# Kernel optimization log

Hardware: AMD Instinct MI355X
Metric: run time of the kernel (lower is better)

The kernel has to match this reference:

```python
import jax, jax.numpy as jnp
import numpy as np

B, L, D = 4096, 50, 128          # users, neighbors/user, embed_dim
N_U, N_I, N_R, N_T = 10000, 100000, 6, 1000
EPS = 1e-5                       # BatchNorm eps (eval mode, running stats)


def setup_inputs() -> dict:
    key = jax.random.key(0)
    ks = iter(jax.random.split(key, 80))
    nk = lambda: next(ks)

    def lin(din, dout):
        s = 1.0 / np.sqrt(din)
        w = jax.random.uniform(nk(), (din, dout), minval=-s, maxval=s, dtype=jnp.float32)
        b = jax.random.uniform(nk(), (dout,), minval=-s, maxval=s, dtype=jnp.float32)
        return w, b

    inp = {}
    # embedding tables (u2e/i2e/r2e/t2e)
    inp['u2e'] = 0.1 * jax.random.normal(nk(), (N_U, D), jnp.float32)
    inp['i2e'] = 0.1 * jax.random.normal(nk(), (N_I, D), jnp.float32)
    inp['r2e'] = 0.1 * jax.random.normal(nk(), (N_R, D), jnp.float32)
    inp['t2e'] = 0.1 * jax.random.normal(nk(), (N_T, D), jnp.float32)
    # neighbor transform MLP
    inp['ne_w'], inp['ne_b'] = lin(3 * D, D)
    inp['ne1_w'], inp['ne1_b'] = lin(D, D)
    # attention MLP (NewAttention: concat(neigh, user) -> D -> D -> 1, softmax over neighbors)
    inp['att1_w'], inp['att1_b'] = lin(2 * D, D)
    inp['att2_w'], inp['att2_b'] = lin(D, D)
    inp['att3_w'], inp['att3_b'] = lin(D, 1)
    # head
    inp['lin_w'], inp['lin_b'] = lin(2 * D, D)
    inp['w1_w'], inp['w1_b'] = lin(D, D // 4)
    inp['bn1_g'] = jnp.ones((D // 4,), jnp.float32)
    inp['bn1_b'] = jnp.zeros((D // 4,), jnp.float32)
    inp['bn1_m'] = 0.1 * jax.random.normal(nk(), (D // 4,), jnp.float32)
    inp['bn1_v'] = jax.random.uniform(nk(), (D // 4,), minval=0.5, maxval=1.5, dtype=jnp.float32)
    inp['w2_w'], inp['w2_b'] = lin(D // 4, D // 8)
    inp['bn2_g'] = jnp.ones((D // 8,), jnp.float32)
    inp['bn2_b'] = jnp.zeros((D // 8,), jnp.float32)
    inp['bn2_m'] = 0.1 * jax.random.normal(nk(), (D // 8,), jnp.float32)
    inp['bn2_v'] = jax.random.uniform(nk(), (D // 8,), minval=0.5, maxval=1.5, dtype=jnp.float32)
    inp['w3_w'], inp['w3_b'] = lin(D // 8, 1)
    # index inputs (padded-fixed neighbor lists)
    inp['user_idx'] = jax.random.randint(nk(), (B,), 0, N_U)
    inp['item_idx'] = jax.random.randint(nk(), (B, L), 0, N_I)
    inp['rat_idx'] = jax.random.randint(nk(), (B, L), 0, N_R)
    inp['time_idx'] = jax.random.randint(nk(), (B, L), 0, N_T)
    return inp


def reference(u2e, i2e, r2e, t2e, ne_w, ne_b, ne1_w, ne1_b,
              att1_w, att1_b, att2_w, att2_b, att3_w, att3_b,
              lin_w, lin_b, w1_w, w1_b, bn1_g, bn1_b, bn1_m, bn1_v,
              w2_w, w2_b, bn2_g, bn2_b, bn2_m, bn2_v, w3_w, w3_b,
              user_idx, item_idx, rat_idx, time_idx):
    u = u2e[user_idx]                                                   # [B, D]
    neigh = jnp.concatenate([i2e[item_idx], r2e[rat_idx], t2e[time_idx]], axis=-1)  # [B, L, 3D]
    x = jax.nn.relu(neigh @ ne_w + ne_b)                                # [B, L, D]
    x = jax.nn.relu(x @ ne1_w + ne1_b)                                  # [B, L, D]
    # attention over neighbors, conditioned on the user embedding
    a = jnp.concatenate([x, jnp.broadcast_to(u[:, None, :], x.shape)], axis=-1)  # [B, L, 2D]
    a = jax.nn.relu(a @ att1_w + att1_b)
    a = jax.nn.relu(a @ att2_w + att2_b)
    att = jax.nn.softmax((a @ att3_w + att3_b)[..., 0], axis=-1)        # [B, L]
    pooled = jnp.einsum('bl,bld->bd', att, x)                           # torch.mm(x.t(), att).t()
    comb = jax.nn.relu(jnp.concatenate([u, pooled], axis=-1) @ lin_w + lin_b)  # [B, D]
    h = comb @ w1_w + w1_b
    h = jax.nn.relu((h - bn1_m) * jax.lax.rsqrt(bn1_v + EPS) * bn1_g + bn1_b)
    h = h @ w2_w + w2_b
    h = jax.nn.relu((h - bn2_m) * jax.lax.rsqrt(bn2_v + EPS) * bn2_g + bn2_b)
    return (h @ w3_w + w3_b)[:, 0]                                      # [B]
```

## Files before the change

kernel.cpp:

```cpp
#include <hip/hip_runtime.h>
#include <hip/hip_bf16.h>

typedef __bf16 bf16x8 __attribute__((ext_vector_type(8)));
typedef float  f32x4  __attribute__((ext_vector_type(4)));

#define W_OFF 0
#define A_OFF 16384
#define X_OFF 29696
#define SMALL 43008
#define SMEM_TOTAL 47104
#define WCHUNK 16384
#define WHALF  8192

#define WS_WPREP 0
#define WS_PI    262144
#define WS_PT    (WS_PI + 25600000)
#define WS_PR    (WS_PT + 512000)
#define WS_PU    (WS_PR + 3072)
#define WS_PU2   (WS_PU + 5120000)

__global__ void prep_weights_kernel(const float* __restrict__ ne_w,
                                    const float* __restrict__ ne1_w,
                                    const float* __restrict__ att1_w,
                                    const float* __restrict__ att2_w,
                                    const float* __restrict__ lin_w,
                                    __hip_bfloat16* __restrict__ wout) {
  __shared__ float tile[64][65];
  const int bx = blockIdx.x;
  const int c = bx >> 2, kt = (bx >> 1) & 1, ntile = bx & 1;
  const float* src; int koff;
  if      (c < 3)  { src = ne_w;   koff = c * 128; }
  else if (c == 3) { src = ne1_w;  koff = 0; }
  else if (c == 4) { src = att1_w; koff = 0; }
  else if (c == 5) { src = att2_w; koff = 0; }
  else if (c == 6) { src = att1_w; koff = 128; }
  else             { src = lin_w;  koff = 0; }
  const int tx = threadIdx.x, ty = threadIdx.y;
#pragma unroll
  for (int r = 0; r < 16; ++r) {
    int k = kt * 64 + r * 4 + ty, n = ntile * 64 + tx;
    tile[r * 4 + ty][tx] = src[(koff + k) * 128 + n];
  }
  __syncthreads();
#pragma unroll
  for (int r = 0; r < 16; ++r) {
    int n = ntile * 64 + r * 4 + ty, k = kt * 64 + tx;
    int h = k >> 6, k64 = k & 63;
    int off = c * WCHUNK + h * WHALF + n * 64 + ((((k64 >> 3) ^ (n & 7))) << 3) + (k64 & 7);
    wout[off] = __float2bfloat16(tile[tx][r * 4 + ty]);
  }
}

__device__ __forceinline__ unsigned short bf_bits(float x) {
  return __builtin_bit_cast(unsigned short, __float2bfloat16(x));
}

__device__ __forceinline__ void mfma_half(const __hip_bfloat16* sIn,
                                          const __hip_bfloat16* sWh,
                                          f32x4 acc[4], int h, int m16, int nh, int lane) {
  const int mr = lane & 15;
  const int kq = lane >> 4;
  const int arow = (m16 * 16 + mr) * 128;
#pragma unroll
  for (int ks = 0; ks < 2; ++ks) {
    const int kb16 = h * 8 + ks * 4 + kq;
    bf16x8 a = *(const bf16x8*)(sIn + arow + ((kb16 ^ mr) << 3));
    const int swzb = (((ks * 4 + kq) ^ (mr & 7)) << 3);
#pragma unroll
    for (int nt = 0; nt < 4; ++nt) {
      const int n = nh * 64 + nt * 16 + mr;
      bf16x8 b = *(const bf16x8*)(sWh + n * 64 + swzb);
      acc[nt] = __builtin_amdgcn_mfma_f32_16x16x32_bf16(a, b, acc[nt], 0, 0, 0);
    }
  }
}

__device__ __forceinline__ void epilogue(f32x4 acc[4], const float* __restrict__ bias,
                                         const float* addvec, __hip_bfloat16* sOut,
                                         int m16, int nh, int lane) {
  const int mr = lane & 15;
  const int rb = m16 * 16 + ((lane >> 4) << 2);
#pragma unroll
  for (int nt = 0; nt < 4; ++nt) {
    const int col = nh * 64 + nt * 16 + mr;
    float bv = bias[col];
    if (addvec) bv += addvec[col];
    const int cblk = col >> 3, clo = col & 7;
#pragma unroll
    for (int r = 0; r < 4; ++r) {
      const int row = rb + r;
      if (row < 50) {
        float v = fmaxf(acc[nt][r] + bv, 0.0f);
        sOut[row * 128 + ((cblk ^ (row & 15)) << 3) + clo] = __float2bfloat16(v);
      }
    }
  }
}

__global__ __launch_bounds__(512) void pgemm_kernel(
    const float* __restrict__ i2e, const float* __restrict__ r2e,
    const float* __restrict__ t2e, const float* __restrict__ u2e,
    const float* __restrict__ ne_b, const __hip_bfloat16* __restrict__ wprep,
    __hip_bfloat16* __restrict__ Pi, float* __restrict__ Pt, float* __restrict__ Pr,
    float* __restrict__ Pu, float* __restrict__ Pu2) {
  __shared__ __align__(16) __hip_bfloat16 sW[WCHUNK];
  __shared__ __align__(16) __hip_bfloat16 sA[64 * 128];
  const int tid = threadIdx.x, lane = tid & 63, wid = tid >> 6;
  const int m16 = wid & 3, nh = wid >> 2;
  const int bx = blockIdx.x;
  const float* src; const __hip_bfloat16* W; float* dst = nullptr;
  const float* addb = nullptr; bool bf_out = false;
  long rows0; int nrows;
  if (bx < 1563)      { src = i2e; W = wprep + 0 * WCHUNK; bf_out = true; rows0 = (long)bx * 64;          nrows = 100000; }
  else if (bx < 1579) { src = t2e; W = wprep + 2 * WCHUNK; dst = Pt;  rows0 = (long)(bx - 1563) * 64; nrows = 1000; }
  else if (bx < 1580) { src = r2e; W = wprep + 1 * WCHUNK; dst = Pr;  rows0 = 0;                      nrows = 6; addb = ne_b; }
  else if (bx < 1737) { src = u2e; W = wprep + 6 * WCHUNK; dst = Pu;  rows0 = (long)(bx - 1580) * 64; nrows = 10000; }
  else                { src = u2e; W = wprep + 7 * WCHUNK; dst = Pu2; rows0 = (long)(bx - 1737) * 64; nrows = 10000; }

#pragma unroll
  for (int i = 0; i < 4; ++i) {
    int g = tid + i * 512;
    __builtin_amdgcn_global_load_lds(
        (__attribute__((address_space(1))) void*)(void*)(W + g * 8),
        (__attribute__((address_space(3))) void*)(void*)(sW + g * 8), 16, 0, 0);
  }
  const float4* s4 = (const float4*)src;
#pragma unroll
  for (int i = 0; i < 2; ++i) {
    int g = tid + i * 512;
    int row = g >> 4, kb = g & 15;
    float4 v0 = {0.f, 0.f, 0.f, 0.f}, v1 = {0.f, 0.f, 0.f, 0.f};
    if (rows0 + row < nrows) {
      long base = (rows0 + row) * 32 + kb * 2;
      v0 = s4[base]; v1 = s4[base + 1];
    }
    uint4 pk;
    pk.x = ((unsigned)bf_bits(v0.y) << 16) | bf_bits(v0.x);
    pk.y = ((unsigned)bf_bits(v0.w) << 16) | bf_bits(v0.z);
    pk.z = ((unsigned)bf_bits(v1.y) << 16) | bf_bits(v1.x);
    pk.w = ((unsigned)bf_bits(v1.w) << 16) | bf_bits(v1.z);
    *(uint4*)(sA + row * 128 + ((kb ^ (row & 15)) << 3)) = pk;
  }
  __syncthreads();

  f32x4 acc[4];
#pragma unroll
  for (int j = 0; j < 4; ++j) acc[j] = (f32x4){0.f, 0.f, 0.f, 0.f};
  mfma_half(sA, sW, acc, 0, m16, nh, lane);
  mfma_half(sA, sW + WHALF, acc, 1, m16, nh, lane);

  const int mr = lane & 15;
  const int rb = m16 * 16 + ((lane >> 4) << 2);
#pragma unroll
  for (int nt = 0; nt < 4; ++nt) {
    const int col = nh * 64 + nt * 16 + mr;
    const float bv = addb ? addb[col] : 0.f;
#pragma unroll
    for (int r = 0; r < 4; ++r) {
      const int row = rb + r;
      if (rows0 + row < nrows) {
        if (bf_out) Pi[(rows0 + row) * 128 + col] = __float2bfloat16(acc[nt][r]);
        else        dst[(rows0 + row) * 128 + col] = acc[nt][r] + bv;
      }
    }
  }
}

__global__ __launch_bounds__(512, 6) void graphdec_main(
    const __hip_bfloat16* __restrict__ Pi, const float* __restrict__ Pt,
    const float* __restrict__ Pr, const float* __restrict__ Pu,
    const float* __restrict__ Pu2,
    const float* __restrict__ ne1_b, const float* __restrict__ att1_b,
    const float* __restrict__ att2_b, const float* __restrict__ att3_w,
    const float* __restrict__ lin_w, const float* __restrict__ lin_b,
    const float* __restrict__ w1_w, const float* __restrict__ w1_b,
    const float* __restrict__ bn1_g, const float* __restrict__ bn1_b,
    const float* __restrict__ bn1_m, const float* __restrict__ bn1_v,
    const float* __restrict__ w2_w, const float* __restrict__ w2_b,
    const float* __restrict__ bn2_g, const float* __restrict__ bn2_b,
    const float* __restrict__ bn2_m, const float* __restrict__ bn2_v,
    const float* __restrict__ w3_w, const float* __restrict__ w3_b,
    const int* __restrict__ user_idx, const int* __restrict__ item_idx,
    const int* __restrict__ rat_idx, const int* __restrict__ time_idx,
    const __hip_bfloat16* __restrict__ wprep, float* __restrict__ out) {
  __shared__ __align__(16) unsigned char smem[SMEM_TOTAL];
  __hip_bfloat16* sW = (__hip_bfloat16*)(smem + W_OFF);
  __hip_bfloat16* sA = (__hip_bfloat16*)(smem + A_OFF);
  __hip_bfloat16* sX = (__hip_bfloat16*)(smem + X_OFF);
  int*   sIdx   = (int*)  (smem + SMALL);
  float* sUatt  = (float*)(smem + SMALL + 768);
  float* sUlin  = (float*)(smem + SMALL + 1280);
  float* sLP0   = (float*)(smem + SMALL + 1792);
  float* sLP1   = (float*)(smem + SMALL + 2048);
  float* sAtt   = (float*)(smem + SMALL + 2304);
  float* sPooled= (float*)(smem + SMALL + 2560);
  float* sComb  = (float*)(smem + SMALL + 3072);
  float* sH1    = (float*)(smem + SMALL + 3584);
  float* sPool4 = (float*)(smem + W_OFF);
  float* sCombP = (float*)(smem + W_OFF + 2048);

  const int tid  = threadIdx.x;
  const int lane = tid & 63;
  const int wid  = tid >> 6;
  const int m16  = wid & 3;
  const int nh   = wid >> 2;
  const int b    = blockIdx.x;

  float att3r[4];
#pragma unroll
  for (int nt = 0; nt < 4; ++nt) att3r[nt] = att3_w[nh * 64 + nt * 16 + (lane & 15)];

  if (tid < 192) {
    int c = tid >> 6, l = tid & 63;
    int v = 0;
    if (l < 50) {
      const int* p = (c == 0) ? item_idx : (c == 1) ? rat_idx : time_idx;
      v = p[b * 50 + l];
    }
    sIdx[tid] = v;
  }
  const int uid = user_idx[b];
  if (tid >= 256 && tid < 384)      sUatt[tid - 256] = Pu [(long)uid * 128 + (tid - 256)];
  else if (tid >= 384)              sUlin[tid - 384] = Pu2[(long)uid * 128 + (tid - 384)];
  __syncthreads();

  auto stage16 = [&](const __hip_bfloat16* __restrict__ src) {
#pragma unroll
    for (int i = 0; i < 2; ++i) {
      int g = tid + i * 512;
      __builtin_amdgcn_global_load_lds(
          (__attribute__((address_space(1))) void*)(void*)(src + g * 8),
          (__attribute__((address_space(3))) void*)(void*)(sW + g * 8), 16, 0, 0);
    }
  };

  f32x4 acc[4];
  const f32x4 zf = {0.f, 0.f, 0.f, 0.f};
  auto zacc = [&]() {
#pragma unroll
    for (int j = 0; j < 4; ++j) acc[j] = zf;
  };

  stage16(wprep + 3 * WCHUNK);
#pragma unroll
  for (int i = 0; i < 2; ++i) {
    int g = tid + i * 512;
    if (g < 832) {
      int row = g >> 4, kb = g & 15;
      uint4 pk = {0u, 0u, 0u, 0u};
      if (row < 50) {
        const bf16x8 pv = *(const bf16x8*)(Pi + (long)sIdx[row] * 128 + kb * 8);
        const float4* pr4 = (const float4*)(Pr + (long)sIdx[64 + row] * 128) + kb * 2;
        const float4* pt4 = (const float4*)(Pt + (long)sIdx[128 + row] * 128) + kb * 2;
        float4 r0 = pr4[0], r1 = pr4[1];
        float4 t0 = pt4[0], t1 = pt4[1];
        float s0 = fmaxf((float)pv[0] + r0.x + t0.x, 0.f);
        float s1 = fmaxf((float)pv[1] + r0.y + t0.y, 0.f);
        float s2 = fmaxf((float)pv[2] + r0.z + t0.z, 0.f);
        float s3 = fmaxf((float)pv[3] + r0.w + t0.w, 0.f);
        float s4 = fmaxf((float)pv[4] + r1.x + t1.x, 0.f);
        float s5 = fmaxf((float)pv[5] + r1.y + t1.y, 0.f);
        float s6 = fmaxf((float)pv[6] + r1.z + t1.z, 0.f);
        float s7 = fmaxf((float)pv[7] + r1.w + t1.w, 0.f);
        pk.x = ((unsigned)bf_bits(s1) << 16) | bf_bits(s0);
        pk.y = ((unsigned)bf_bits(s3) << 16) | bf_bits(s2);
        pk.z = ((unsigned)bf_bits(s5) << 16) | bf_bits(s4);
        pk.w = ((unsigned)bf_bits(s7) << 16) | bf_bits(s6);
      }
      *(uint4*)(sA + row * 128 + ((kb ^ (row & 15)) << 3)) = pk;
    }
  }
  __syncthreads();

  zacc();
  mfma_half(sA, sW, acc, 0, m16, nh, lane);
  __syncthreads();
  stage16(wprep + 3 * WCHUNK + WHALF);
  __syncthreads();
  mfma_half(sA, sW, acc, 1, m16, nh, lane);
  __syncthreads();
  stage16(wprep + 4 * WCHUNK);
  epilogue(acc, ne1_b, nullptr, sX, m16, nh, lane);
  __syncthreads();

  zacc();
  mfma_half(sX, sW, acc, 0, m16, nh, lane);
  __syncthreads();
  stage16(wprep + 4 * WCHUNK + WHALF);
  __syncthreads();
  mfma_half(sX, sW, acc, 1, m16, nh, lane);
  __syncthreads();
  stage16(wprep + 5 * WCHUNK);
  epilogue(acc, att1_b, sUatt, sA, m16, nh, lane);
  __syncthreads();

  zacc();
  mfma_half(sA, sW, acc, 0, m16, nh, lane);
  __syncthreads();
  stage16(wprep + 5 * WCHUNK + WHALF);
  __syncthreads();
  mfma_half(sA, sW, acc, 1, m16, nh, lane);
  {
    float lp[4] = {0.f, 0.f, 0.f, 0.f};
#pragma unroll
    for (int nt = 0; nt < 4; ++nt) {
      const int col = nh * 64 + nt * 16 + (lane & 15);
      const float b2 = att2_b[col];
#pragma unroll
      for (int r = 0; r < 4; ++r)
        lp[r] += fmaxf(acc[nt][r] + b2, 0.f) * att3r[nt];
    }
#pragma unroll
    for (int off = 1; off < 16; off <<= 1) {
#pragma unroll
      for (int r = 0; r < 4; ++r) lp[r] += __shfl_xor(lp[r], off);
    }
    if ((lane & 15) == 0) {
      const int rowb = m16 * 16 + ((lane >> 4) << 2);
      float* dst = nh ? sLP1 : sLP0;
#pragma unroll
      for (int r = 0; r < 4; ++r) dst[rowb + r] = lp[r];
    }
  }
  __syncthreads();

  if (wid == 0) {
    float v = (lane < 50) ? (sLP0[lane] + sLP1[lane]) : -3.4e38f;
    float m = v;
    for (int off = 32; off > 0; off >>= 1) m = fmaxf(m, __shfl_xor(m, off));
    float e = (lane < 50) ? __expf(v - m) : 0.f;
    float s = e;
    for (int off = 32; off > 0; off >>= 1) s += __shfl_xor(s, off);
    sAtt[lane] = e / s;
  }
  __syncthreads();

  {
    int q = tid >> 7, d = tid & 127;
    const int cblk = d >> 3, clo = d & 7;
    float s = 0.f;
    for (int l = q; l < 50; l += 4)
      s += sAtt[l] * (float)sX[l * 128 + ((cblk ^ (l & 15)) << 3) + clo];
    sPool4[q * 128 + d] = s;
  }
  __syncthreads();
  if (tid < 128)
    sPooled[tid] = sPool4[tid] + sPool4[128 + tid] + sPool4[256 + tid] + sPool4[384 + tid];
  __syncthreads();

  {
    int q = tid >> 7, d = tid & 127;
    float s = 0.f;
    for (int j = q * 32; j < q * 32 + 32; ++j) s += sPooled[j] * lin_w[(128 + j) * 128 + d];
    sCombP[q * 128 + d] = s;
  }
  __syncthreads();
  if (tid < 128)
    sComb[tid] = fmaxf(sCombP[tid] + sCombP[128 + tid] + sCombP[256 + tid] + sCombP[384 + tid]
                       + sUlin[tid] + lin_b[tid], 0.f);
  __syncthreads();

  if (wid == 0) {
    if (lane < 32) {
      float s = w1_b[lane];
      for (int k = 0; k < 128; ++k) s += sComb[k] * w1_w[k * 32 + lane];
      s = (s - bn1_m[lane]) * rsqrtf(bn1_v[lane] + 1e-5f) * bn1_g[lane] + bn1_b[lane];
      sH1[lane] = fmaxf(s, 0.f);
    }
    if (lane < 16) {
      float s = w2_b[lane];
      for (int k = 0; k < 32; ++k) s += sH1[k] * w2_w[k * 16 + lane];
      s = (s - bn2_m[lane]) * rsqrtf(bn2_v[lane] + 1e-5f) * bn2_g[lane] + bn2_b[lane];
      float p = fmaxf(s, 0.f) * w3_w[lane];
      p += __shfl_xor(p, 1); p += __shfl_xor(p, 2);
      p += __shfl_xor(p, 4); p += __shfl_xor(p, 8);
      if (lane == 0) out[b] = p + w3_b[0];
    }
  }
}

extern "C" void kernel_launch(void* const* d_in, const int* in_sizes, int n_in,
                              void* d_out, int out_size, void* d_ws, size_t ws_size,
                              hipStream_t stream) {
  const float* u2e    = (const float*)d_in[0];
  const float* i2e    = (const float*)d_in[1];
  const float* r2e    = (const float*)d_in[2];
  const float* t2e    = (const float*)d_in[3];
  const float* ne_w   = (const float*)d_in[4];
  const float* ne_b   = (const float*)d_in[5];
  const float* ne1_w  = (const float*)d_in[6];
  const float* ne1_b  = (const float*)d_in[7];
  const float* att1_w = (const float*)d_in[8];
  const float* att1_b = (const float*)d_in[9];
  const float* att2_w = (const float*)d_in[10];
  const float* att2_b = (const float*)d_in[11];
  const float* att3_w = (const float*)d_in[12];
  const float* att3_b = (const float*)d_in[13];
  const float* lin_w  = (const float*)d_in[14];
  const float* lin_b  = (const float*)d_in[15];
  const float* w1_w   = (const float*)d_in[16];
  const float* w1_b   = (const float*)d_in[17];
  const float* bn1_g  = (const float*)d_in[18];
  const float* bn1_b  = (const float*)d_in[19];
  const float* bn1_m  = (const float*)d_in[20];
  const float* bn1_v  = (const float*)d_in[21];
  const float* w2_w   = (const float*)d_in[22];
  const float* w2_b   = (const float*)d_in[23];
  const float* bn2_g  = (const float*)d_in[24];
  const float* bn2_b  = (const float*)d_in[25];
  const float* bn2_m  = (const float*)d_in[26];
  const float* bn2_v  = (const float*)d_in[27];
  const float* w3_w   = (const float*)d_in[28];
  const float* w3_b   = (const float*)d_in[29];
  const int* user_idx = (const int*)d_in[30];
  const int* item_idx = (const int*)d_in[31];
  const int* rat_idx  = (const int*)d_in[32];
  const int* time_idx = (const int*)d_in[33];
  (void)att3_b;

  char* ws = (char*)d_ws;
  __hip_bfloat16* wprep = (__hip_bfloat16*)(ws + WS_WPREP);
  __hip_bfloat16* Pi = (__hip_bfloat16*)(ws + WS_PI);
  float* Pt  = (float*)(ws + WS_PT);
  float* Pr  = (float*)(ws + WS_PR);
  float* Pu  = (float*)(ws + WS_PU);
  float* Pu2 = (float*)(ws + WS_PU2);
  float* out = (float*)d_out;

  prep_weights_kernel<<<32, dim3(64, 4), 0, stream>>>(ne_w, ne1_w, att1_w, att2_w,
                                                      lin_w, wprep);
  pgemm_kernel<<<1894, 512, 0, stream>>>(i2e, r2e, t2e, u2e, ne_b, wprep,
                                         Pi, Pt, Pr, Pu, Pu2);
  graphdec_main<<<4096, 512, 0, stream>>>(
      Pi, Pt, Pr, Pu, Pu2, ne1_b, att1_b, att2_b, att3_w,
      lin_w, lin_b, w1_w, w1_b, bn1_g, bn1_b, bn1_m, bn1_v, w2_w, w2_b,
      bn2_g, bn2_b, bn2_m, bn2_v, w3_w, w3_b,
      user_idx, item_idx, rat_idx, time_idx, wprep, out);
}
```

Baseline: 242.3 us.

## Process two users per 1024-thread block sharing staged weight chunks

Fuses two users into one 1024-thread block. Each half-block gets its own activation, hidden and scratch LDS regions, while the bf16 weight chunk staged into LDS is shared by both, so each weight chunk is loaded once per two users. It also drops the zero-fill of padding rows 50-63 in the gather stage, cutting the activation buffers to 50 rows. The trade-off is a larger LDS footprint per block and a tighter register budget from the launch bounds. Reading the unwritten pad rows could also touch the other user's buffer unless those rows are masked later.

```diff
diff --git a/kernel.cpp b/kernel.cpp
--- a/kernel.cpp
+++ b/kernel.cpp
@@ -5,10 +5,10 @@
 typedef float  f32x4  __attribute__((ext_vector_type(4)));
 
 #define W_OFF 0
-#define A_OFF 16384
-#define X_OFF 29696
-#define SMALL 43008
-#define SMEM_TOTAL 47104
+#define ABUF  16384
+#define XBUF  41984
+#define SMALL 67584
+#define SMEM_TOTAL 75776
 #define WCHUNK 16384
 #define WHALF  8192
 
@@ -166,7 +166,7 @@
   }
 }
 
-__global__ __launch_bounds__(512, 6) void graphdec_main(
+__global__ __launch_bounds__(1024, 8) void graphdec_main(
     const __hip_bfloat16* __restrict__ Pi, const float* __restrict__ Pt,
     const float* __restrict__ Pr, const float* __restrict__ Pu,
     const float* __restrict__ Pu2,
@@ -184,54 +184,54 @@
     const int* __restrict__ rat_idx, const int* __restrict__ time_idx,
     const __hip_bfloat16* __restrict__ wprep, float* __restrict__ out) {
   __shared__ __align__(16) unsigned char smem[SMEM_TOTAL];
-  __hip_bfloat16* sW = (__hip_bfloat16*)(smem + W_OFF);
-  __hip_bfloat16* sA = (__hip_bfloat16*)(smem + A_OFF);
-  __hip_bfloat16* sX = (__hip_bfloat16*)(smem + X_OFF);
-  int*   sIdx   = (int*)  (smem + SMALL);
-  float* sUatt  = (float*)(smem + SMALL + 768);
-  float* sUlin  = (float*)(smem + SMALL + 1280);
-  float* sLP0   = (float*)(smem + SMALL + 1792);
-  float* sLP1   = (float*)(smem + SMALL + 2048);
-  float* sAtt   = (float*)(smem + SMALL + 2304);
-  float* sPooled= (float*)(smem + SMALL + 2560);
-  float* sComb  = (float*)(smem + SMALL + 3072);
-  float* sH1    = (float*)(smem + SMALL + 3584);
-  float* sPool4 = (float*)(smem + W_OFF);
-  float* sCombP = (float*)(smem + W_OFF + 2048);
-
   const int tid  = threadIdx.x;
+  const int t    = tid & 511;
+  const int u    = tid >> 9;
   const int lane = tid & 63;
-  const int wid  = tid >> 6;
+  const int wid  = (tid >> 6) & 7;
   const int m16  = wid & 3;
   const int nh   = wid >> 2;
   const int b    = blockIdx.x;
+  const long ub  = (long)b * 2 + u;
+
+  __hip_bfloat16* sW = (__hip_bfloat16*)(smem + W_OFF);
+  __hip_bfloat16* sA = (__hip_bfloat16*)(smem + ABUF + u * 12800);
+  __hip_bfloat16* sX = (__hip_bfloat16*)(smem + XBUF + u * 12800);
+  unsigned char* sSm = smem + SMALL + u * 4096;
+  int*   sIdx   = (int*)  sSm;
+  float* sUatt  = (float*)(sSm + 768);
+  float* sUlin  = (float*)(sSm + 1280);
+  float* sLP0   = (float*)(sSm + 1792);
+  float* sLP1   = (float*)(sSm + 2048);
+  float* sAtt   = (float*)(sSm + 2304);
+  float* sPooled= (float*)(sSm + 2560);
+  float* sComb  = (float*)(sSm + 3072);
+  float* sH1    = (float*)(sSm + 3584);
+  float* sPool4 = (float*)(smem + W_OFF + u * 4096);
+  float* sCombP = (float*)(smem + W_OFF + u * 4096 + 2048);
 
   float att3r[4];
 #pragma unroll
   for (int nt = 0; nt < 4; ++nt) att3r[nt] = att3_w[nh * 64 + nt * 16 + (lane & 15)];
 
-  if (tid < 192) {
-    int c = tid >> 6, l = tid & 63;
+  if (t < 192) {
+    int c = t >> 6, l = t & 63;
     int v = 0;
     if (l < 50) {
       const int* p = (c == 0) ? item_idx : (c == 1) ? rat_idx : time_idx;
-      v = p[b * 50 + l];
-    }
-    sIdx[tid] = v;
-  }
-  const int uid = user_idx[b];
-  if (tid >= 256 && tid < 384)      sUatt[tid - 256] = Pu [(long)uid * 128 + (tid - 256)];
-  else if (tid >= 384)              sUlin[tid - 384] = Pu2[(long)uid * 128 + (tid - 384)];
+      v = p[ub * 50 + l];
+    }
+    sIdx[t] = v;
+  }
+  const int uid = user_idx[ub];
+  if (t >= 256 && t < 384)      sUatt[t - 256] = Pu [(long)uid * 128 + (t - 256)];
+  else if (t >= 384)            sUlin[t - 384] = Pu2[(long)uid * 128 + (t - 384)];
   __syncthreads();
 
   auto stage16 = [&](const __hip_bfloat16* __restrict__ src) {
-#pragma unroll
-    for (int i = 0; i < 2; ++i) {
-      int g = tid + i * 512;
-      __builtin_amdgcn_global_load_lds(
-          (__attribute__((address_space(1))) void*)(void*)(src + g * 8),
-          (__attribute__((address_space(3))) void*)(void*)(sW + g * 8), 16, 0, 0);
-    }
+    __builtin_amdgcn_global_load_lds(
+        (__attribute__((address_space(1))) void*)(void*)(src + tid * 8),
+        (__attribute__((address_space(3))) void*)(void*)(sW + tid * 8), 16, 0, 0);
   };
 
   f32x4 acc[4];
@@ -244,29 +244,27 @@
   stage16(wprep + 3 * WCHUNK);
 #pragma unroll
   for (int i = 0; i < 2; ++i) {
-    int g = tid + i * 512;
-    if (g < 832) {
+    int g = t + i * 512;
+    if (g < 800) {
       int row = g >> 4, kb = g & 15;
-      uint4 pk = {0u, 0u, 0u, 0u};
-      if (row < 50) {
-        const bf16x8 pv = *(const bf16x8*)(Pi + (long)sIdx[row] * 128 + kb * 8);
-        const float4* pr4 = (const float4*)(Pr + (long)sIdx[64 + row] * 128) + kb * 2;
-        const float4* pt4 = (const float4*)(Pt + (long)sIdx[128 + row] * 128) + kb * 2;
-        float4 r0 = pr4[0], r1 = pr4[1];
-        float4 t0 = pt4[0], t1 = pt4[1];
-        float s0 = fmaxf((float)pv[0] + r0.x + t0.x, 0.f);
-        float s1 = fmaxf((float)pv[1] + r0.y + t0.y, 0.f);
-        float s2 = fmaxf((float)pv[2] + r0.z + t0.z, 0.f);
-        float s3 = fmaxf((float)pv[3] + r0.w + t0.w, 0.f);
-        float s4 = fmaxf((float)pv[4] + r1.x + t1.x, 0.f);
-        float s5 = fmaxf((float)pv[5] + r1.y + t1.y, 0.f);
-        float s6 = fmaxf((float)pv[6] + r1.z + t1.z, 0.f);
-        float s7 = fmaxf((float)pv[7] + r1.w + t1.w, 0.f);
-        pk.x = ((unsigned)bf_bits(s1) << 16) | bf_bits(s0);
-        pk.y = ((unsigned)bf_bits(s3) << 16) | bf_bits(s2);
-        pk.z = ((unsigned)bf_bits(s5) << 16) | bf_bits(s4);
-        pk.w = ((unsigned)bf_bits(s7) << 16) | bf_bits(s6);
-      }
+      const bf16x8 pv = *(const bf16x8*)(Pi + (long)sIdx[row] * 128 + kb * 8);
+      const float4* pr4 = (const float4*)(Pr + (long)sIdx[64 + row] * 128) + kb * 2;
+      const float4* pt4 = (const float4*)(Pt + (long)sIdx[128 + row] * 128) + kb * 2;
+      float4 r0 = pr4[0], r1 = pr4[1];
+      float4 t0 = pt4[0], t1 = pt4[1];
+      float s0 = fmaxf((float)pv[0] + r0.x + t0.x, 0.f);
+      float s1 = fmaxf((float)pv[1] + r0.y + t0.y, 0.f);
+      float s2 = fmaxf((float)pv[2] + r0.z + t0.z, 0.f);
+      float s3 = fmaxf((float)pv[3] + r0.w + t0.w, 0.f);
+      float s4 = fmaxf((float)pv[4] + r1.x + t1.x, 0.f);
+      float s5 = fmaxf((float)pv[5] + r1.y + t1.y, 0.f);
+      float s6 = fmaxf((float)pv[6] + r1.z + t1.z, 0.f);
+      float s7 = fmaxf((float)pv[7] + r1.w + t1.w, 0.f);
+      uint4 pk;
+      pk.x = ((unsigned)bf_bits(s1) << 16) | bf_bits(s0);
+      pk.y = ((unsigned)bf_bits(s3) << 16) | bf_bits(s2);
+      pk.z = ((unsigned)bf_bits(s5) << 16) | bf_bits(s4);
+      pk.w = ((unsigned)bf_bits(s7) << 16) | bf_bits(s6);
       *(uint4*)(sA + row * 128 + ((kb ^ (row & 15)) << 3)) = pk;
     }
   }
@@ -336,7 +334,7 @@
   __syncthreads();
 
   {
-    int q = tid >> 7, d = tid & 127;
+    int q = t >> 7, d = t & 127;
     const int cblk = d >> 3, clo = d & 7;
     float s = 0.f;
     for (int l = q; l < 50; l += 4)
@@ -344,20 +342,20 @@
     sPool4[q * 128 + d] = s;
   }
   __syncthreads();
-  if (tid < 128)
-    sPooled[tid] = sPool4[tid] + sPool4[128 + tid] + sPool4[256 + tid] + sPool4[384 + tid];
+  if (t < 128)
+    sPooled[t] = sPool4[t] + sPool4[128 + t] + sPool4[256 + t] + sPool4[384 + t];
   __syncthreads();
 
   {
-    int q = tid >> 7, d = tid & 127;
+    int q = t >> 7, d = t & 127;
     float s = 0.f;
     for (int j = q * 32; j < q * 32 + 32; ++j) s += sPooled[j] * lin_w[(128 + j) * 128 + d];
     sCombP[q * 128 + d] = s;
   }
   __syncthreads();
-  if (tid < 128)
-    sComb[tid] = fmaxf(sCombP[tid] + sCombP[128 + tid] + sCombP[256 + tid] + sCombP[384 + tid]
-                       + sUlin[tid] + lin_b[tid], 0.f);
+  if (t < 128)
+    sComb[t] = fmaxf(sCombP[t] + sCombP[128 + t] + sCombP[256 + t] + sCombP[384 + t]
+                     + sUlin[t] + lin_b[t], 0.f);
   __syncthreads();
 
   if (wid == 0) {
@@ -374,7 +372,7 @@
       float p = fmaxf(s, 0.f) * w3_w[lane];
       p += __shfl_xor(p, 1); p += __shfl_xor(p, 2);
       p += __shfl_xor(p, 4); p += __shfl_xor(p, 8);
-      if (lane == 0) out[b] = p + w3_b[0];
+      if (lane == 0) out[ub] = p + w3_b[0];
     }
   }
 }
@@ -431,7 +429,7 @@
                                                       lin_w, wprep);
   pgemm_kernel<<<1894, 512, 0, stream>>>(i2e, r2e, t2e, u2e, ne_b, wprep,
                                          Pi, Pt, Pr, Pu, Pu2);
-  graphdec_main<<<4096, 512, 0, stream>>>(
+  graphdec_main<<<2048, 1024, 0, stream>>>(
       Pi, Pt, Pr, Pu, Pu2, ne1_b, att1_b, att2_b, att3_w,
       lin_w, lin_b, w1_w, w1_b, bn1_g, bn1_b, bn1_m, bn1_v, w2_w, w2_b,
       bn2_g, bn2_b, bn2_m, bn2_v, w3_w, w3_b,
```

Result: slower. 283.9 us (+17.2%).

## Process four row tiles per pgemm block with register-prefetched next tile

Applied to the files above, without the earlier changes.

Each pgemm block now loops over up to four 64-row tiles instead of handling one. The weight chunk is loaded into LDS once per block, and the next tile's global loads are issued into registers while the current tile's MFMA and stores run. The aim is to amortize weight staging and block launch overhead and to hide global load latency. In exchange the grid shrinks from 1894 to 476 blocks, which lowers parallelism on a large GPU, and each tile step adds two extra barriers.

```diff
diff --git a/kernel.cpp b/kernel.cpp
--- a/kernel.cpp
+++ b/kernel.cpp
@@ -110,12 +110,14 @@
   const int bx = blockIdx.x;
   const float* src; const __hip_bfloat16* W; float* dst = nullptr;
   const float* addb = nullptr; bool bf_out = false;
-  long rows0; int nrows;
-  if (bx < 1563)      { src = i2e; W = wprep + 0 * WCHUNK; bf_out = true; rows0 = (long)bx * 64;          nrows = 100000; }
-  else if (bx < 1579) { src = t2e; W = wprep + 2 * WCHUNK; dst = Pt;  rows0 = (long)(bx - 1563) * 64; nrows = 1000; }
-  else if (bx < 1580) { src = r2e; W = wprep + 1 * WCHUNK; dst = Pr;  rows0 = 0;                      nrows = 6; addb = ne_b; }
-  else if (bx < 1737) { src = u2e; W = wprep + 6 * WCHUNK; dst = Pu;  rows0 = (long)(bx - 1580) * 64; nrows = 10000; }
-  else                { src = u2e; W = wprep + 7 * WCHUNK; dst = Pu2; rows0 = (long)(bx - 1737) * 64; nrows = 10000; }
+  long rows0; long nrows;
+  if (bx < 391)      { src = i2e; W = wprep + 0 * WCHUNK; bf_out = true; rows0 = (long)bx * 256;        nrows = 100000; }
+  else if (bx < 395) { src = t2e; W = wprep + 2 * WCHUNK; dst = Pt;  rows0 = (long)(bx - 391) * 256; nrows = 1000; }
+  else if (bx < 396) { src = r2e; W = wprep + 1 * WCHUNK; dst = Pr;  rows0 = 0;                      nrows = 6; addb = ne_b; }
+  else if (bx < 436) { src = u2e; W = wprep + 6 * WCHUNK; dst = Pu;  rows0 = (long)(bx - 396) * 256; nrows = 10000; }
+  else               { src = u2e; W = wprep + 7 * WCHUNK; dst = Pu2; rows0 = (long)(bx - 436) * 256; nrows = 10000; }
+  int T = (int)((nrows - rows0 + 63) >> 6);
+  if (T > 4) T = 4;
 
 #pragma unroll
   for (int i = 0; i < 4; ++i) {
@@ -124,44 +126,77 @@
         (__attribute__((address_space(1))) void*)(void*)(W + g * 8),
         (__attribute__((address_space(3))) void*)(void*)(sW + g * 8), 16, 0, 0);
   }
+
   const float4* s4 = (const float4*)src;
-#pragma unroll
-  for (int i = 0; i < 2; ++i) {
-    int g = tid + i * 512;
-    int row = g >> 4, kb = g & 15;
-    float4 v0 = {0.f, 0.f, 0.f, 0.f}, v1 = {0.f, 0.f, 0.f, 0.f};
-    if (rows0 + row < nrows) {
-      long base = (rows0 + row) * 32 + kb * 2;
-      v0 = s4[base]; v1 = s4[base + 1];
-    }
-    uint4 pk;
-    pk.x = ((unsigned)bf_bits(v0.y) << 16) | bf_bits(v0.x);
-    pk.y = ((unsigned)bf_bits(v0.w) << 16) | bf_bits(v0.z);
-    pk.z = ((unsigned)bf_bits(v1.y) << 16) | bf_bits(v1.x);
-    pk.w = ((unsigned)bf_bits(v1.w) << 16) | bf_bits(v1.z);
-    *(uint4*)(sA + row * 128 + ((kb ^ (row & 15)) << 3)) = pk;
-  }
-  __syncthreads();
-
-  f32x4 acc[4];
-#pragma unroll
-  for (int j = 0; j < 4; ++j) acc[j] = (f32x4){0.f, 0.f, 0.f, 0.f};
-  mfma_half(sA, sW, acc, 0, m16, nh, lane);
-  mfma_half(sA, sW + WHALF, acc, 1, m16, nh, lane);
+  const int row = (tid & 511) >> 4;
+
+  auto load_tile = [&](int tt, float4 v[4]) {
+#pragma unroll
+    for (int i = 0; i < 2; ++i) {
+      int g = tid + i * 512;
+      int rr = g >> 4, kb = g & 15;
+      v[i * 2 + 0] = (float4){0.f, 0.f, 0.f, 0.f};
+      v[i * 2 + 1] = (float4){0.f, 0.f, 0.f, 0.f};
+      long gr = rows0 + (long)tt * 64 + rr;
+      if (gr < nrows) {
+        long base = gr * 32 + kb * 2;
+        v[i * 2 + 0] = s4[base];
+        v[i * 2 + 1] = s4[base + 1];
+      }
+    }
+  };
+  auto tile_to_lds = [&](const float4 v[4]) {
+#pragma unroll
+    for (int i = 0; i < 2; ++i) {
+      int g = tid + i * 512;
+      int rr = g >> 4, kb = g & 15;
+      uint4 pk;
+      pk.x = ((unsigned)bf_bits(v[i * 2].y) << 16) | bf_bits(v[i * 2].x);
+      pk.y = ((unsigned)bf_bits(v[i * 2].w) << 16) | bf_bits(v[i * 2].z);
+      pk.z = ((unsigned)bf_bits(v[i * 2 + 1].y) << 16) | bf_bits(v[i * 2 + 1].x);
+      pk.w = ((unsigned)bf_bits(v[i * 2 + 1].w) << 16) | bf_bits(v[i * 2 + 1].z);
+      *(uint4*)(sA + rr * 128 + ((kb ^ (rr & 15)) << 3)) = pk;
+    }
+  };
+  (void)row;
+
+  {
+    float4 cur[4];
+    load_tile(0, cur);
+    tile_to_lds(cur);
+  }
+  __syncthreads();
 
   const int mr = lane & 15;
   const int rb = m16 * 16 + ((lane >> 4) << 2);
-#pragma unroll
-  for (int nt = 0; nt < 4; ++nt) {
-    const int col = nh * 64 + nt * 16 + mr;
-    const float bv = addb ? addb[col] : 0.f;
-#pragma unroll
-    for (int r = 0; r < 4; ++r) {
-      const int row = rb + r;
-      if (rows0 + row < nrows) {
-        if (bf_out) Pi[(rows0 + row) * 128 + col] = __float2bfloat16(acc[nt][r]);
-        else        dst[(rows0 + row) * 128 + col] = acc[nt][r] + bv;
+  for (int t = 0; t < T; ++t) {
+    float4 nxt[4];
+    if (t + 1 < T) load_tile(t + 1, nxt);
+
+    f32x4 acc[4];
+#pragma unroll
+    for (int j = 0; j < 4; ++j) acc[j] = (f32x4){0.f, 0.f, 0.f, 0.f};
+    mfma_half(sA, sW, acc, 0, m16, nh, lane);
+    mfma_half(sA, sW + WHALF, acc, 1, m16, nh, lane);
+
+#pragma unroll
+    for (int nt = 0; nt < 4; ++nt) {
+      const int col = nh * 64 + nt * 16 + mr;
+      const float bv = addb ? addb[col] : 0.f;
+#pragma unroll
+      for (int r = 0; r < 4; ++r) {
+        long gr = rows0 + (long)t * 64 + rb + r;
+        if (gr < nrows) {
+          if (bf_out) Pi[gr * 128 + col] = __float2bfloat16(acc[nt][r]);
+          else        dst[gr * 128 + col] = acc[nt][r] + bv;
+        }
       }
+    }
+
+    if (t + 1 < T) {
+      __syncthreads();
+      tile_to_lds(nxt);
+      __syncthreads();
     }
   }
 }
@@ -429,8 +464,8 @@
 
   prep_weights_kernel<<<32, dim3(64, 4), 0, stream>>>(ne_w, ne1_w, att1_w, att2_w,
                                                       lin_w, wprep);
-  pgemm_kernel<<<1894, 512, 0, stream>>>(i2e, r2e, t2e, u2e, ne_b, wprep,
-                                         Pi, Pt, Pr, Pu, Pu2);
+  pgemm_kernel<<<476, 512, 0, stream>>>(i2e, r2e, t2e, u2e, ne_b, wprep,
+                                        Pi, Pt, Pr, Pu, Pu2);
   graphdec_main<<<4096, 512, 0, stream>>>(
       Pi, Pt, Pr, Pu, Pu2, ne1_b, att1_b, att2_b, att3_w,
       lin_w, lin_b, w1_w, w1_b, bn1_g, bn1_b, bn1_m, bn1_v, w2_w, w2_b,
```

Result: slower. 254.6 us (+5.1%).

## Make main kernel persistent and prefetch next user's indices and weights during tail

Applied to the files above, without the earlier changes.

The main kernel becomes persistent with 768 blocks looping over the 4096 users. It double-buffers the per-user index and user-projection buffers in shared memory. During each user's softmax, pooling and head work it prefetches the next user's first weight chunk and its indices, hiding launch and startup latency. The pool scratch moves from the weight region to the activation region so the weight prefetch does not clash with it. Fewer blocks may lower the parallelism available to hide gather latency, and the shared layout grows slightly.

```diff
diff --git a/kernel.cpp b/kernel.cpp
--- a/kernel.cpp
+++ b/kernel.cpp
@@ -7,8 +7,16 @@
 #define W_OFF 0
 #define A_OFF 16384
 #define X_OFF 29696
-#define SMALL 43008
-#define SMEM_TOTAL 47104
+#define S_IDX   43008
+#define S_UATT  44544
+#define S_ULIN  45568
+#define S_LP0   46592
+#define S_LP1   46848
+#define S_ATT   47104
+#define S_POOL  47360
+#define S_COMB  47872
+#define S_H1    48384
+#define SMEM_TOTAL 48640
 #define WCHUNK 16384
 #define WHALF  8192
 
@@ -187,42 +195,27 @@
   __hip_bfloat16* sW = (__hip_bfloat16*)(smem + W_OFF);
   __hip_bfloat16* sA = (__hip_bfloat16*)(smem + A_OFF);
   __hip_bfloat16* sX = (__hip_bfloat16*)(smem + X_OFF);
-  int*   sIdx   = (int*)  (smem + SMALL);
-  float* sUatt  = (float*)(smem + SMALL + 768);
-  float* sUlin  = (float*)(smem + SMALL + 1280);
-  float* sLP0   = (float*)(smem + SMALL + 1792);
-  float* sLP1   = (float*)(smem + SMALL + 2048);
-  float* sAtt   = (float*)(smem + SMALL + 2304);
-  float* sPooled= (float*)(smem + SMALL + 2560);
-  float* sComb  = (float*)(smem + SMALL + 3072);
-  float* sH1    = (float*)(smem + SMALL + 3584);
-  float* sPool4 = (float*)(smem + W_OFF);
-  float* sCombP = (float*)(smem + W_OFF + 2048);
+  int*   sIdxB  = (int*)  (smem + S_IDX);
+  float* sUattB = (float*)(smem + S_UATT);
+  float* sUlinB = (float*)(smem + S_ULIN);
+  float* sLP0   = (float*)(smem + S_LP0);
+  float* sLP1   = (float*)(smem + S_LP1);
+  float* sAtt   = (float*)(smem + S_ATT);
+  float* sPooled= (float*)(smem + S_POOL);
+  float* sComb  = (float*)(smem + S_COMB);
+  float* sH1    = (float*)(smem + S_H1);
+  float* sPool4 = (float*)(smem + A_OFF);
+  float* sCombP = (float*)(smem + A_OFF + 2048);
 
   const int tid  = threadIdx.x;
   const int lane = tid & 63;
   const int wid  = tid >> 6;
   const int m16  = wid & 3;
   const int nh   = wid >> 2;
-  const int b    = blockIdx.x;
 
   float att3r[4];
 #pragma unroll
   for (int nt = 0; nt < 4; ++nt) att3r[nt] = att3_w[nh * 64 + nt * 16 + (lane & 15)];
-
-  if (tid < 192) {
-    int c = tid >> 6, l = tid & 63;
-    int v = 0;
-    if (l < 50) {
-      const int* p = (c == 0) ? item_idx : (c == 1) ? rat_idx : time_idx;
-      v = p[b * 50 + l];
-    }
-    sIdx[tid] = v;
-  }
-  const int uid = user_idx[b];
-  if (tid >= 256 && tid < 384)      sUatt[tid - 256] = Pu [(long)uid * 128 + (tid - 256)];
-  else if (tid >= 384)              sUlin[tid - 384] = Pu2[(long)uid * 128 + (tid - 384)];
-  __syncthreads();
 
   auto stage16 = [&](const __hip_bfloat16* __restrict__ src) {
 #pragma unroll
@@ -241,140 +234,190 @@
     for (int j = 0; j < 4; ++j) acc[j] = zf;
   };
 
-  stage16(wprep + 3 * WCHUNK);
-#pragma unroll
-  for (int i = 0; i < 2; ++i) {
-    int g = tid + i * 512;
-    if (g < 832) {
-      int row = g >> 4, kb = g & 15;
-      uint4 pk = {0u, 0u, 0u, 0u};
-      if (row < 50) {
-        const bf16x8 pv = *(const bf16x8*)(Pi + (long)sIdx[row] * 128 + kb * 8);
-        const float4* pr4 = (const float4*)(Pr + (long)sIdx[64 + row] * 128) + kb * 2;
-        const float4* pt4 = (const float4*)(Pt + (long)sIdx[128 + row] * 128) + kb * 2;
-        float4 r0 = pr4[0], r1 = pr4[1];
-        float4 t0 = pt4[0], t1 = pt4[1];
-        float s0 = fmaxf((float)pv[0] + r0.x + t0.x, 0.f);
-        float s1 = fmaxf((float)pv[1] + r0.y + t0.y, 0.f);
-        float s2 = fmaxf((float)pv[2] + r0.z + t0.z, 0.f);
-        float s3 = fmaxf((float)pv[3] + r0.w + t0.w, 0.f);
-        float s4 = fmaxf((float)pv[4] + r1.x + t1.x, 0.f);
-        float s5 = fmaxf((float)pv[5] + r1.y + t1.y, 0.f);
-        float s6 = fmaxf((float)pv[6] + r1.z + t1.z, 0.f);
-        float s7 = fmaxf((float)pv[7] + r1.w + t1.w, 0.f);
-        pk.x = ((unsigned)bf_bits(s1) << 16) | bf_bits(s0);
-        pk.y = ((unsigned)bf_bits(s3) << 16) | bf_bits(s2);
-        pk.z = ((unsigned)bf_bits(s5) << 16) | bf_bits(s4);
-        pk.w = ((unsigned)bf_bits(s7) << 16) | bf_bits(s6);
-      }
-      *(uint4*)(sA + row * 128 + ((kb ^ (row & 15)) << 3)) = pk;
-    }
-  }
-  __syncthreads();
-
-  zacc();
-  mfma_half(sA, sW, acc, 0, m16, nh, lane);
-  __syncthreads();
-  stage16(wprep + 3 * WCHUNK + WHALF);
-  __syncthreads();
-  mfma_half(sA, sW, acc, 1, m16, nh, lane);
-  __syncthreads();
-  stage16(wprep + 4 * WCHUNK);
-  epilogue(acc, ne1_b, nullptr, sX, m16, nh, lane);
-  __syncthreads();
-
-  zacc();
-  mfma_half(sX, sW, acc, 0, m16, nh, lane);
-  __syncthreads();
-  stage16(wprep + 4 * WCHUNK + WHALF);
-  __syncthreads();
-  mfma_half(sX, sW, acc, 1, m16, nh, lane);
-  __syncthreads();
-  stage16(wprep + 5 * WCHUNK);
-  epilogue(acc, att1_b, sUatt, sA, m16, nh, lane);
-  __syncthreads();
-
-  zacc();
-  mfma_half(sA, sW, acc, 0, m16, nh, lane);
-  __syncthreads();
-  stage16(wprep + 5 * WCHUNK + WHALF);
-  __syncthreads();
-  mfma_half(sA, sW, acc, 1, m16, nh, lane);
+  long u = blockIdx.x;
   {
-    float lp[4] = {0.f, 0.f, 0.f, 0.f};
-#pragma unroll
-    for (int nt = 0; nt < 4; ++nt) {
-      const int col = nh * 64 + nt * 16 + (lane & 15);
-      const float b2 = att2_b[col];
-#pragma unroll
-      for (int r = 0; r < 4; ++r)
-        lp[r] += fmaxf(acc[nt][r] + b2, 0.f) * att3r[nt];
-    }
-#pragma unroll
-    for (int off = 1; off < 16; off <<= 1) {
-#pragma unroll
-      for (int r = 0; r < 4; ++r) lp[r] += __shfl_xor(lp[r], off);
-    }
-    if ((lane & 15) == 0) {
-      const int rowb = m16 * 16 + ((lane >> 4) << 2);
-      float* dst = nh ? sLP1 : sLP0;
-#pragma unroll
-      for (int r = 0; r < 4; ++r) dst[rowb + r] = lp[r];
-    }
-  }
-  __syncthreads();
-
-  if (wid == 0) {
-    float v = (lane < 50) ? (sLP0[lane] + sLP1[lane]) : -3.4e38f;
-    float m = v;
-    for (int off = 32; off > 0; off >>= 1) m = fmaxf(m, __shfl_xor(m, off));
-    float e = (lane < 50) ? __expf(v - m) : 0.f;
-    float s = e;
-    for (int off = 32; off > 0; off >>= 1) s += __shfl_xor(s, off);
-    sAtt[lane] = e / s;
-  }
-  __syncthreads();
-
-  {
-    int q = tid >> 7, d = tid & 127;
-    const int cblk = d >> 3, clo = d & 7;
-    float s = 0.f;
-    for (int l = q; l < 50; l += 4)
-      s += sAtt[l] * (float)sX[l * 128 + ((cblk ^ (l & 15)) << 3) + clo];
-    sPool4[q * 128 + d] = s;
-  }
-  __syncthreads();
-  if (tid < 128)
-    sPooled[tid] = sPool4[tid] + sPool4[128 + tid] + sPool4[256 + tid] + sPool4[384 + tid];
-  __syncthreads();
-
-  {
-    int q = tid >> 7, d = tid & 127;
-    float s = 0.f;
-    for (int j = q * 32; j < q * 32 + 32; ++j) s += sPooled[j] * lin_w[(128 + j) * 128 + d];
-    sCombP[q * 128 + d] = s;
-  }
-  __syncthreads();
-  if (tid < 128)
-    sComb[tid] = fmaxf(sCombP[tid] + sCombP[128 + tid] + sCombP[256 + tid] + sCombP[384 + tid]
-                       + sUlin[tid] + lin_b[tid], 0.f);
-  __syncthreads();
-
-  if (wid == 0) {
-    if (lane < 32) {
-      float s = w1_b[lane];
-      for (int k = 0; k < 128; ++k) s += sComb[k] * w1_w[k * 32 + lane];
-      s = (s - bn1_m[lane]) * rsqrtf(bn1_v[lane] + 1e-5f) * bn1_g[lane] + bn1_b[lane];
-      sH1[lane] = fmaxf(s, 0.f);
-    }
-    if (lane < 16) {
-      float s = w2_b[lane];
-      for (int k = 0; k < 32; ++k) s += sH1[k] * w2_w[k * 16 + lane];
-      s = (s - bn2_m[lane]) * rsqrtf(bn2_v[lane] + 1e-5f) * bn2_g[lane] + bn2_b[lane];
-      float p = fmaxf(s, 0.f) * w3_w[lane];
-      p += __shfl_xor(p, 1); p += __shfl_xor(p, 2);
-      p += __shfl_xor(p, 4); p += __shfl_xor(p, 8);
-      if (lane == 0) out[b] = p + w3_b[0];
+    if (tid < 192) {
+      int c = tid >> 6, l = tid & 63;
+      int v = 0;
+      if (l < 50) {
+        const int* p = (c == 0) ? item_idx : (c == 1) ? rat_idx : time_idx;
+        v = p[u * 50 + l];
+      }
+      sIdxB[tid] = v;
+    }
+    const int uid = user_idx[u];
+    if (tid >= 256 && tid < 384)      sUattB[tid - 256] = Pu [(long)uid * 128 + (tid - 256)];
+    else if (tid >= 384)              sUlinB[tid - 384] = Pu2[(long)uid * 128 + (tid - 384)];
+    stage16(wprep + 3 * WCHUNK);
+  }
+
+  for (int it = 0; u < 4096; u += gridDim.x, ++it) {
+    const int p = it & 1;
+    const int*   sIdx  = sIdxB  + p * 192;
+    const float* sUatt = sUattB + p * 128;
+    const float* sUlin = sUlinB + p * 128;
+    __syncthreads();
+
+#pragma unroll
+    for (int i = 0; i < 2; ++i) {
+      int g = tid + i * 512;
+      if (g < 832) {
+        int row = g >> 4, kb = g & 15;
+        uint4 pk = {0u, 0u, 0u, 0u};
+        if (row < 50) {
+          const bf16x8 pv = *(const bf16x8*)(Pi + (long)sIdx[row] * 128 + kb * 8);
+          const float4* pr4 = (const float4*)(Pr + (long)sIdx[64 + row] * 128) + kb * 2;
+          const float4* pt4 = (const float4*)(Pt + (long)sIdx[128 + row] * 128) + kb * 2;
+          float4 r0 = pr4[0], r1 = pr4[1];
+          float4 t0 = pt4[0], t1 = pt4[1];
+          float s0 = fmaxf((float)pv[0] + r0.x + t0.x, 0.f);
+          float s1 = fmaxf((float)pv[1] + r0.y + t0.y, 0.f);
+          float s2 = fmaxf((float)pv[2] + r0.z + t0.z, 0.f);
+          float s3 = fmaxf((float)pv[3] + r0.w + t0.w, 0.f);
+          float s4 = fmaxf((float)pv[4] + r1.x + t1.x, 0.f);
+          float s5 = fmaxf((float)pv[5] + r1.y + t1.y, 0.f);
+          float s6 = fmaxf((float)pv[6] + r1.z + t1.z, 0.f);
+          float s7 = fmaxf((float)pv[7] + r1.w + t1.w, 0.f);
+          pk.x = ((unsigned)bf_bits(s1) << 16) | bf_bits(s0);
+          pk.y = ((unsigned)bf_bits(s3) << 16) | bf_bits(s2);
+          pk.z = ((unsigned)bf_bits(s5) << 16) | bf_bits(s4);
+          pk.w = ((unsigned)bf_bits(s7) << 16) | bf_bits(s6);
+        }
+        *(uint4*)(sA + row * 128 + ((kb ^ (row & 15)) << 3)) = pk;
+      }
+    }
+    __syncthreads();
+
+    zacc();
+    mfma_half(sA, sW, acc, 0, m16, nh, lane);
+    __syncthreads();
+    stage16(wprep + 3 * WCHUNK + WHALF);
+    __syncthreads();
+    mfma_half(sA, sW, acc, 1, m16, nh, lane);
+    __syncthreads();
+    stage16(wprep + 4 * WCHUNK);
+    epilogue(acc, ne1_b, nullptr, sX, m16, nh, lane);
+    __syncthreads();
+
+    zacc();
+    mfma_half(sX, sW, acc, 0, m16, nh, lane);
+    __syncthreads();
+    stage16(wprep + 4 * WCHUNK + WHALF);
+    __syncthreads();
+    mfma_half(sX, sW, acc, 1, m16, nh, lane);
+    __syncthreads();
+    stage16(wprep + 5 * WCHUNK);
+    epilogue(acc, att1_b, sUatt, sA, m16, nh, lane);
+    __syncthreads();
+
+    zacc();
+    mfma_half(sA, sW, acc, 0, m16, nh, lane);
+    __syncthreads();
+    stage16(wprep + 5 * WCHUNK + WHALF);
+    __syncthreads();
+    mfma_half(sA, sW, acc, 1, m16, nh, lane);
+    {
+      float lp[4] = {0.f, 0.f, 0.f, 0.f};
+#pragma unroll
+      for (int nt = 0; nt < 4; ++nt) {
+        const int col = nh * 64 + nt * 16 + (lane & 15);
+        const float b2 = att2_b[col];
+#pragma unroll
+        for (int r = 0; r < 4; ++r)
+          lp[r] += fmaxf(acc[nt][r] + b2, 0.f) * att3r[nt];
+      }
+#pragma unroll
+      for (int off = 1; off < 16; off <<= 1) {
+#pragma unroll
+        for (int r = 0; r < 4; ++r) lp[r] += __shfl_xor(lp[r], off);
+      }
+      if ((lane & 15) == 0) {
+        const int rowb = m16 * 16 + ((lane >> 4) << 2);
+        float* dst = nh ? sLP1 : sLP0;
+#pragma unroll
+        for (int r = 0; r < 4; ++r) dst[rowb + r] = lp[r];
+      }
+    }
+    __syncthreads();
+
+    const long nu = u + gridDim.x;
+    const bool more = nu < 4096;
+    if (more) stage16(wprep + 3 * WCHUNK);
+    int pv = 0; float puv = 0.f, pu2v = 0.f;
+    if (more) {
+      if (tid < 192) {
+        int c = tid >> 6, l = tid & 63;
+        if (l < 50) {
+          const int* pp = (c == 0) ? item_idx : (c == 1) ? rat_idx : time_idx;
+          pv = pp[nu * 50 + l];
+        }
+      }
+      const int nuid = user_idx[nu];
+      if (tid >= 256 && tid < 384)      puv  = Pu [(long)nuid * 128 + (tid - 256)];
+      else if (tid >= 384)              pu2v = Pu2[(long)nuid * 128 + (tid - 384)];
+    }
+
+    if (wid == 0) {
+      float v = (lane < 50) ? (sLP0[lane] + sLP1[lane]) : -3.4e38f;
+      float m = v;
+      for (int off = 32; off > 0; off >>= 1) m = fmaxf(m, __shfl_xor(m, off));
+      float e = (lane < 50) ? __expf(v - m) : 0.f;
+      float s = e;
+      for (int off = 32; off > 0; off >>= 1) s += __shfl_xor(s, off);
+      sAtt[lane] = e / s;
+    }
+    __syncthreads();
+
+    {
+      int q = tid >> 7, d = tid & 127;
+      const int cblk = d >> 3, clo = d & 7;
+      float s = 0.f;
+      for (int l = q; l < 50; l += 4)
+        s += sAtt[l] * (float)sX[l * 128 + ((cblk ^ (l & 15)) << 3) + clo];
+      sPool4[q * 128 + d] = s;
+    }
+    __syncthreads();
+    if (tid < 128)
+      sPooled[tid] = sPool4[tid] + sPool4[128 + tid] + sPool4[256 + tid] + sPool4[384 + tid];
+    __syncthreads();
+
+    {
+      int q = tid >> 7, d = tid & 127;
+      float s = 0.f;
+      for (int j = q * 32; j < q * 32 + 32; ++j) s += sPooled[j] * lin_w[(128 + j) * 128 + d];
+      sCombP[q * 128 + d] = s;
+    }
+    __syncthreads();
+
+    if (more) {
+      int*   nIdx  = sIdxB  + (p ^ 1) * 192;
+      float* nUatt = sUattB + (p ^ 1) * 128;
+      float* nUlin = sUlinB + (p ^ 1) * 128;
+      if (tid < 192) nIdx[tid] = pv;
+      if (tid >= 256 && tid < 384)      nUatt[tid - 256] = puv;
+      else if (tid >= 384)              nUlin[tid - 384] = pu2v;
+    }
+    if (tid < 128)
+      sComb[tid] = fmaxf(sCombP[tid] + sCombP[128 + tid] + sCombP[256 + tid] + sCombP[384 + tid]
+                         + sUlin[tid] + lin_b[tid], 0.f);
+    __syncthreads();
+
+    if (wid == 0) {
+      if (lane < 32) {
+        float s = w1_b[lane];
+        for (int k = 0; k < 128; ++k) s += sComb[k] * w1_w[k * 32 + lane];
+        s = (s - bn1_m[lane]) * rsqrtf(bn1_v[lane] + 1e-5f) * bn1_g[lane] + bn1_b[lane];
+        sH1[lane] = fmaxf(s, 0.f);
+      }
+      if (lane < 16) {
+        float s = w2_b[lane];
+        for (int k = 0; k < 32; ++k) s += sH1[k] * w2_w[k * 16 + lane];
+        s = (s - bn2_m[lane]) * rsqrtf(bn2_v[lane] + 1e-5f) * bn2_g[lane] + bn2_b[lane];
+        float q = fmaxf(s, 0.f) * w3_w[lane];
+        q += __shfl_xor(q, 1); q += __shfl_xor(q, 2);
+        q += __shfl_xor(q, 4); q += __shfl_xor(q, 8);
+        if (lane == 0) out[u] = q + w3_b[0];
+      }
     }
   }
 }
@@ -431,7 +474,7 @@
                                                       lin_w, wprep);
   pgemm_kernel<<<1894, 512, 0, stream>>>(i2e, r2e, t2e, u2e, ne_b, wprep,
                                          Pi, Pt, Pr, Pu, Pu2);
-  graphdec_main<<<4096, 512, 0, stream>>>(
+  graphdec_main<<<768, 512, 0, stream>>>(
       Pi, Pt, Pr, Pu, Pu2, ne1_b, att1_b, att2_b, att3_w,
       lin_w, lin_b, w1_w, w1_b, bn1_g, bn1_b, bn1_m, bn1_v, w2_w, w2_b,
       bn2_g, bn2_b, bn2_m, bn2_v, w3_w, w3_b,
```

Result: slower. 639.2 us (+163.8%).
